# Kernel optimization log

Hardware: AMD Instinct MI355X
Metric: run time of the kernel (lower is better)

## Reference

```python
import itertools
import jax, jax.numpy as jnp
import numpy as np

B, N, F = 128, 128, 64  # batch, n_nodes, feat

def _edge_indices(n_nodes, receiving=True):
    # itertools.permutations(range(n), 2) ordering, matching the original layer
    pairs = np.array(list(itertools.permutations(range(n_nodes), 2)), dtype=np.int32)
    return pairs[:, 0] if receiving else pairs[:, 1]  # [n_edges]

def setup_inputs() -> dict:
    key = jax.random.key(0)
    x = jax.random.normal(key, (B, N, F), dtype=jnp.float32)
    return {"x": x}

def reference(x) -> jnp.ndarray:
    # node_to_edge=True, receiving=True: adjacency[0, i, r]=1 selects receiver node
    # of edge i; dense matmul A @ x is exactly a gather x[:, idx, :].
    n_nodes = x.shape[-2]
    idx = jnp.asarray(_edge_indices(n_nodes, receiving=True))  # [n_edges]
    return jnp.take(x, idx, axis=-2)  # [B, n_edges, F]
```

## Files before the change

### kernel.cpp

```cpp
#include <hip/hip_runtime.h>


typedef float f32x4 __attribute__((ext_vector_type(4)));

constexpr unsigned Bn = 128;
constexpr unsigned Nn = 128;
constexpr unsigned Fn = 64;
constexpr unsigned NE = Nn * (Nn - 1);
constexpr unsigned F4 = Fn / 4;

__global__ __launch_bounds__(256) void node_edge_bcast(
    const f32x4* __restrict__ x, f32x4* __restrict__ out) {
    const unsigned blk  = blockIdx.x;
    const unsigned tid  = threadIdx.x;
    const unsigned f4   = tid & (F4 - 1);
    const unsigned row0 = tid >> 4;

    const f32x4 v = x[blk * F4 + f4];

    const unsigned b    = blk >> 7;
    const unsigned node = blk & (Nn - 1);
    f32x4* dst = out + (b * NE + node * (Nn - 1)) * F4;

    #pragma unroll
    for (unsigned r = row0; r < Nn - 1; r += 16) {
        __builtin_nontemporal_store(v, &dst[r * F4 + f4]);
    }
}

extern "C" void kernel_launch(void* const* d_in, const int* in_sizes, int n_in,
                              void* d_out, int out_size, void* d_ws, size_t ws_size,
                              hipStream_t stream) {
    const f32x4* x = (const f32x4*)d_in[0];
    f32x4* out = (f32x4*)d_out;

    node_edge_bcast<<<Bn * Nn, 256, 0, stream>>>(x, out);
}
```

Measured before the change: 103.1 us.

## Restructure broadcast into per-wave streams of consecutive nodes with fewer blocks

Replaces the one-block-per-node launch (16384 blocks) with 256 blocks of 4 waves, where each wave preloads 16 consecutive node rows into registers and writes each one 127 times as a contiguous stream. Nontemporal stores are replaced with regular stores. The intent is to cut block scheduling overhead and produce long sequential write streams per wave. The cost is that only 1024 waves cover a 256-CU GPU, which may underfill the memory pipeline, and regular stores may pollute the cache.

```diff
diff --git a/kernel.cpp b/kernel.cpp
--- a/kernel.cpp
+++ b/kernel.cpp
@@ -3,28 +3,35 @@
 
 typedef float f32x4 __attribute__((ext_vector_type(4)));
 
-constexpr unsigned Bn = 128;
-constexpr unsigned Nn = 128;
-constexpr unsigned Fn = 64;
-constexpr unsigned NE = Nn * (Nn - 1);
-constexpr unsigned F4 = Fn / 4;
+constexpr unsigned Nn  = 128;
+constexpr unsigned REP = Nn - 1;
+constexpr unsigned F4  = 16;
+constexpr unsigned NPW = 16;
+constexpr unsigned WAVES = 1024;
 
-__global__ __launch_bounds__(256) void node_edge_bcast(
+__global__ __launch_bounds__(256) void node_edge_streams(
     const f32x4* __restrict__ x, f32x4* __restrict__ out) {
-    const unsigned blk  = blockIdx.x;
     const unsigned tid  = threadIdx.x;
-    const unsigned f4   = tid & (F4 - 1);
-    const unsigned row0 = tid >> 4;
+    const unsigned lane = tid & 63;
+    const unsigned wid  = blockIdx.x * 4 + (tid >> 6);
+    const unsigned f4   = lane & (F4 - 1);
+    const unsigned rg0  = lane >> 4;
 
-    const f32x4 v = x[blk * F4 + f4];
+    const unsigned pair0 = wid * NPW;
 
-    const unsigned b    = blk >> 7;
-    const unsigned node = blk & (Nn - 1);
-    f32x4* dst = out + (b * NE + node * (Nn - 1)) * F4;
+    f32x4 v[NPW];
+    #pragma unroll
+    for (unsigned n = 0; n < NPW; ++n)
+        v[n] = x[(pair0 + n) * F4 + f4];
 
+    f32x4* dst = out + (size_t)pair0 * REP * F4 + f4;
     #pragma unroll
-    for (unsigned r = row0; r < Nn - 1; r += 16) {
-        __builtin_nontemporal_store(v, &dst[r * F4 + f4]);
+    for (unsigned n = 0; n < NPW; ++n) {
+        f32x4* dn = dst + n * REP * F4;
+        #pragma unroll 8
+        for (unsigned r = rg0; r < REP; r += 4) {
+            dn[r * F4] = v[n];
+        }
     }
 }
 
@@ -34,5 +41,5 @@
     const f32x4* x = (const f32x4*)d_in[0];
     f32x4* out = (f32x4*)d_out;
 
-    node_edge_bcast<<<Bn * Nn, 256, 0, stream>>>(x, out);
+    node_edge_streams<<<WAVES / 4, 256, 0, stream>>>(x, out);
 }
```

Result: slower. 119.7 us (+16.1%).

## Replace per-node broadcast with grid-stride gather using software-pipelined loads

Applied to the files above, without the earlier changes.

Swaps the one-block-per-node broadcast kernel for a persistent grid of 256x256 threads. Each thread walks the output in grid-stride order, computes the source index with integer div/mod, and keeps two loads in flight ahead of each store. The aim is to cut launch and block-scheduling overhead and overlap reads with writes. In exchange it re-reads x for every output element instead of once per node, adds division arithmetic, uses only 256 blocks, and drops the nontemporal stores.

```diff
diff --git a/kernel.cpp b/kernel.cpp
--- a/kernel.cpp
+++ b/kernel.cpp
@@ -5,27 +5,40 @@
 
 constexpr unsigned Bn = 128;
 constexpr unsigned Nn = 128;
-constexpr unsigned Fn = 64;
 constexpr unsigned NE = Nn * (Nn - 1);
-constexpr unsigned F4 = Fn / 4;
+constexpr unsigned F4 = 16;
+constexpr unsigned TOTAL4 = Bn * NE * F4;
+constexpr unsigned NTH = 256 * 256;
+constexpr unsigned ITERS = TOTAL4 / NTH;
 
-__global__ __launch_bounds__(256) void node_edge_bcast(
+__device__ __forceinline__ unsigned src_index(unsigned o) {
+    unsigned f4   = o & (F4 - 1);
+    unsigned rest = o >> 4;
+    unsigned e    = rest % NE;
+    unsigned b    = rest / NE;
+    unsigned node = e / (Nn - 1);
+    return (b * Nn + node) * F4 + f4;
+}
+
+__global__ __launch_bounds__(256) void node_edge_gs_pipe(
     const f32x4* __restrict__ x, f32x4* __restrict__ out) {
-    const unsigned blk  = blockIdx.x;
-    const unsigned tid  = threadIdx.x;
-    const unsigned f4   = tid & (F4 - 1);
-    const unsigned row0 = tid >> 4;
+    const unsigned t = blockIdx.x * 256 + threadIdx.x;
 
-    const f32x4 v = x[blk * F4 + f4];
+    f32x4 v0 = x[src_index(t)];
+    f32x4 v1 = x[src_index(t + NTH)];
 
-    const unsigned b    = blk >> 7;
-    const unsigned node = blk & (Nn - 1);
-    f32x4* dst = out + (b * NE + node * (Nn - 1)) * F4;
-
-    #pragma unroll
-    for (unsigned r = row0; r < Nn - 1; r += 16) {
-        __builtin_nontemporal_store(v, &dst[r * F4 + f4]);
+    unsigned o = t;
+    #pragma unroll 2
+    for (unsigned k = 0; k < ITERS - 2; ++k) {
+        f32x4 vn = x[src_index(o + 2 * NTH)];
+        out[o] = v0;
+        v0 = v1;
+        v1 = vn;
+        o += NTH;
     }
+    out[o] = v0;
+    o += NTH;
+    out[o] = v1;
 }
 
 extern "C" void kernel_launch(void* const* d_in, const int* in_sizes, int n_in,
@@ -34,5 +47,5 @@
     const f32x4* x = (const f32x4*)d_in[0];
     f32x4* out = (f32x4*)d_out;
 
-    node_edge_bcast<<<Bn * Nn, 256, 0, stream>>>(x, out);
+    node_edge_gs_pipe<<<256, 256, 0, stream>>>(x, out);
 }
```

Result: slower. 197.3 us (+91.3%).

## Use persistent blocks that each process 64 node rows sequentially with prefetch

Applied to the files above, without the earlier changes.

Replaces the one-block-per-(batch,node) grid of 16384 blocks with 256 blocks, each looping over 64 consecutive (batch,node) pairs. The next input row is prefetched while the current one is being stored. Stores also change from nontemporal to regular stores. This cuts block launch overhead, but 256 blocks may be too few to saturate write bandwidth on a large GPU.

```diff
diff --git a/kernel.cpp b/kernel.cpp
--- a/kernel.cpp
+++ b/kernel.cpp
@@ -3,28 +3,36 @@
 
 typedef float f32x4 __attribute__((ext_vector_type(4)));
 
-constexpr unsigned Bn = 128;
-constexpr unsigned Nn = 128;
-constexpr unsigned Fn = 64;
-constexpr unsigned NE = Nn * (Nn - 1);
-constexpr unsigned F4 = Fn / 4;
+constexpr unsigned Nn   = 128;
+constexpr unsigned REP  = Nn - 1;
+constexpr unsigned F4   = 16;
+constexpr unsigned PAIRS = 128 * 128;
+constexpr unsigned PPB  = PAIRS / 256;
 
-__global__ __launch_bounds__(256) void node_edge_bcast(
+__global__ __launch_bounds__(256) void node_edge_seq(
     const f32x4* __restrict__ x, f32x4* __restrict__ out) {
-    const unsigned blk  = blockIdx.x;
     const unsigned tid  = threadIdx.x;
     const unsigned f4   = tid & (F4 - 1);
-    const unsigned row0 = tid >> 4;
+    const unsigned row  = tid >> 4;
 
-    const f32x4 v = x[blk * F4 + f4];
+    const unsigned pair0 = blockIdx.x * PPB;
 
-    const unsigned b    = blk >> 7;
-    const unsigned node = blk & (Nn - 1);
-    f32x4* dst = out + (b * NE + node * (Nn - 1)) * F4;
+    f32x4 v = x[pair0 * F4 + f4];
 
-    #pragma unroll
-    for (unsigned r = row0; r < Nn - 1; r += 16) {
-        __builtin_nontemporal_store(v, &dst[r * F4 + f4]);
+    f32x4* dst = out + (size_t)pair0 * REP * F4;
+
+    for (unsigned p = 0; p < PPB; ++p) {
+        f32x4 vnext;
+        if (p + 1 < PPB) vnext = x[(pair0 + p + 1) * F4 + f4];
+
+        f32x4* dp = dst + (size_t)p * REP * F4 + row * F4 + f4;
+        #pragma unroll
+        for (unsigned j = 0; j < 8; ++j) {
+            unsigned r = j * 16 + row;
+            if (r < REP) dp[j * 16 * F4] = v;
+        }
+
+        v = vnext;
     }
 }
 
@@ -34,5 +42,5 @@
     const f32x4* x = (const f32x4*)d_in[0];
     f32x4* out = (f32x4*)d_out;
 
-    node_edge_bcast<<<Bn * Nn, 256, 0, stream>>>(x, out);
+    node_edge_seq<<<256, 256, 0, stream>>>(x, out);
 }
```

New measurement: 106.0 us. 2.8% more time.
